# Performance work log

Measured on AMD Instinct MI355X. Metric: run time of the kernel, lower is better.

Reference implementation:

```python
import jax, jax.numpy as jnp
import numpy as np
from jax import lax

EPS = 1e-9

def _squash(v):
    # v: [..., D]; squash nonlinearity from CapsNet
    n = jnp.sum(jnp.square(v), axis=-1, keepdims=True)
    return (n / (1.0 + n) / jnp.sqrt(n + EPS)) * v

def setup_inputs() -> dict:
    key = jax.random.key(0)
    ks = jax.random.split(key, 12)
    B, S, D, NI = 1024, 200, 64, 4
    N_UID, N_MID = 50000, 100000
    return {
        "uid": jax.random.randint(ks[0], (B,), 0, N_UID, dtype=jnp.int32),
        "age": jax.random.randint(ks[1], (B,), 0, N_UID, dtype=jnp.int32),
        "gender": jax.random.randint(ks[2], (B,), 0, N_UID, dtype=jnp.int32),
        "occup": jax.random.randint(ks[3], (B,), 0, N_UID, dtype=jnp.int32),
        "mid_his": jax.random.randint(ks[4], (B, S), 0, N_MID, dtype=jnp.int32),
        "mask": jax.random.randint(ks[5], (B, S), 0, 2).astype(jnp.float32),
        "user_emb_table": jax.random.normal(ks[6], (N_UID, D), jnp.float32) * 0.1,
        "age_table": jax.random.normal(ks[7], (N_UID, D), jnp.float32) * 0.1,
        "gender_table": jax.random.normal(ks[8], (N_UID, D), jnp.float32) * 0.1,
        "occup_table": jax.random.normal(ks[9], (N_UID, D), jnp.float32) * 0.1,
        "mid_emb_table": jax.random.normal(ks[10], (N_MID, D), jnp.float32) * 0.1,
        "w_capsule": jax.random.normal(ks[11], (S, NI * D, D), jnp.float32),
    }

def reference(uid, age, gender, occup, mid_his, mask,
              user_emb_table, age_table, gender_table, occup_table,
              mid_emb_table, w_capsule):
    NI = 4
    B, S = mid_his.shape
    D = mid_emb_table.shape[1]

    # user profile: mean of 4 stacked user feature embeddings
    user_profile = (user_emb_table[uid] + gender_table[gender]
                    + age_table[age] + occup_table[occup]) * 0.25  # [B,D]

    # masked item history embeddings
    item_his = mid_emb_table[mid_his] * mask[:, :, None]  # [B,S,D]

    # adjacency: sigmoid(sum_d h_i[d]*h_j[d]*u[d]) without [B,S,S,D] blowup
    hu = item_his * user_profile[:, None, :]              # [B,S,D]
    adj = jax.nn.sigmoid(jnp.einsum('bid,bjd->bij', hu, item_his))  # [B,S,S]
    adj = adj * mask[:, None, :] * mask[:, :, None]

    # --- CapsuleNetwork, bilinear_type=2 ---
    # TF: sum(w[1,S,NI*D,D] * u[B,S,1,D], axis=3) == contraction over D
    hat = jnp.einsum('bsd,sed->bse', item_his, w_capsule)  # [B,S,NI*D]
    hat = hat.reshape(B, S, NI, D).transpose(0, 2, 1, 3)   # [B,NI,S,D]
    hat_iter = lax.stop_gradient(hat)

    cw = jnp.zeros((B, NI, S), dtype=item_his.dtype)  # routing logits
    atten_mask = mask[:, None, :]                     # [B,1,S] broadcast over NI
    for i in range(3):
        sw = jax.nn.softmax(cw, axis=1)               # softmax over interests
        sw = jnp.where(atten_mask == 0, 0.0, sw)      # [B,NI,S]
        if i < 2:
            cap = _squash(jnp.einsum('bks,bksd->bkd', sw, hat_iter))  # [B,NI,D]
            delta = jnp.einsum('bksd,bkd->bks', hat_iter, cap)
            cw = cw + delta
        else:
            cap = _squash(jnp.einsum('bks,bksd->bkd', sw, hat))
    interest_capsule = cap  # [B,NI,D]; relu_layer=False -> no projection
    return interest_capsule, adj
```

## Files before the change

### kernel.cpp

```cpp
#include <hip/hip_runtime.h>

#define B_SZ 1024
#define S_SZ 200
#define D_SZ 64
#define NI_SZ 4
#define E_SZ 256

using u16 = unsigned short;
using u32 = unsigned int;
typedef short  sh4    __attribute__((ext_vector_type(4)));
typedef short  sh8    __attribute__((ext_vector_type(8)));
typedef __bf16 bf16x8 __attribute__((ext_vector_type(8)));
typedef float  f32x4  __attribute__((ext_vector_type(4)));

__device__ __forceinline__ u16 f2bf(float x) {
  u32 u = __float_as_uint(x);
  u += 0x7FFFu + ((u >> 16) & 1u);
  return (u16)(u >> 16);
}
__device__ __forceinline__ float bf2f(u16 h) {
  return __uint_as_float(((u32)h) << 16);
}
__device__ __forceinline__ sh8 ldsr(const u16* arr, int row, int kshort) {
  const int idx = row * 64 + (kshort ^ ((row & 7) << 3));
  return *(const sh8*)(arr + idx);
}
__device__ __forceinline__ bf16x8 ldsw(const u16* arr, int row, int kshort) {
  return __builtin_bit_cast(bf16x8, ldsr(arr, row, kshort));
}
__device__ __forceinline__ void stsw(u16* arr, int row, int c, sh8 v) {
  *(sh8*)(arr + row * 64 + 8 * (c ^ (row & 7))) = v;
}
__device__ __forceinline__ sh8 cvt8(const float* __restrict__ src, float m) {
  const float4 a = *(const float4*)(src);
  const float4 d = *(const float4*)(src + 4);
  sh8 v;
  v[0] = (short)f2bf(a.x * m); v[1] = (short)f2bf(a.y * m);
  v[2] = (short)f2bf(a.z * m); v[3] = (short)f2bf(a.w * m);
  v[4] = (short)f2bf(d.x * m); v[5] = (short)f2bf(d.y * m);
  v[6] = (short)f2bf(d.z * m); v[7] = (short)f2bf(d.w * m);
  return v;
}

__global__ __launch_bounds__(256) void adj_kernel(
    const int* __restrict__ uid, const int* __restrict__ age,
    const int* __restrict__ gender, const int* __restrict__ occup,
    const float* __restrict__ U, const float* __restrict__ AT,
    const float* __restrict__ GT, const float* __restrict__ OT,
    const int* __restrict__ mid_his, const float* __restrict__ mask,
    const float* __restrict__ memb, float* __restrict__ adj)
{
  const int b = blockIdx.x;
  __shared__ u16   Hs[208 * 64];
  __shared__ float Ms[208];
  __shared__ int   midS[S_SZ];
  __shared__ float pS[D_SZ];
  const int tid = threadIdx.x;

  if (tid < 208) Ms[tid] = (tid < S_SZ) ? mask[b * S_SZ + tid] : 0.f;
  if (tid < S_SZ) midS[tid] = mid_his[b * S_SZ + tid];
  if (tid < D_SZ) {
    float v = U[(size_t)uid[b]     * D_SZ + tid]
            + GT[(size_t)gender[b] * D_SZ + tid]
            + AT[(size_t)age[b]    * D_SZ + tid]
            + OT[(size_t)occup[b]  * D_SZ + tid];
    pS[tid] = 0.25f * v;
  }
  __syncthreads();

  for (int idx = tid; idx < S_SZ * 8; idx += 256) {
    const int row = idx >> 3, c = idx & 7;
    const float m = Ms[row];
    sh8 v = {0, 0, 0, 0, 0, 0, 0, 0};
    if (m != 0.f) v = cvt8(memb + (size_t)midS[row] * D_SZ + c * 8, m);
    stsw(Hs, row, c, v);
  }
  if (tid < 64) {
    sh8 z = {0,0,0,0,0,0,0,0};
    stsw(Hs, S_SZ + (tid >> 3), tid & 7, z);
  }
  __syncthreads();

  const int w = tid >> 6, l = tid & 63;
  const int lr = l & 15, lg = l >> 4;
  float pvA[8], pvB[8];
  #pragma unroll
  for (int j = 0; j < 8; j++) { pvA[j] = pS[lg * 8 + j]; pvB[j] = pS[32 + lg * 8 + j]; }

  float* outb = adj + (size_t)b * S_SZ * S_SZ;
  for (int mt = 0; mt < 13; mt++) {
    const int arow = mt * 16 + lr;
    const sh8 r0 = ldsr(Hs, arow, lg * 8);
    const sh8 r1 = ldsr(Hs, arow, 32 + lg * 8);
    sh8 h0, h1;
    #pragma unroll
    for (int j = 0; j < 8; j++) {
      h0[j] = (short)f2bf(bf2f((u16)r0[j]) * pvA[j]);
      h1[j] = (short)f2bf(bf2f((u16)r1[j]) * pvB[j]);
    }
    const bf16x8 a0 = __builtin_bit_cast(bf16x8, h0);
    const bf16x8 a1 = __builtin_bit_cast(bf16x8, h1);
    for (int nt = w; nt < 13; nt += 4) {
      const int brow = nt * 16 + lr;
      const bf16x8 b0 = ldsw(Hs, brow, lg * 8);
      const bf16x8 b1 = ldsw(Hs, brow, 32 + lg * 8);
      f32x4 acc = {0.f, 0.f, 0.f, 0.f};
      acc = __builtin_amdgcn_mfma_f32_16x16x32_bf16(a0, b0, acc, 0, 0, 0);
      acc = __builtin_amdgcn_mfma_f32_16x16x32_bf16(a1, b1, acc, 0, 0, 0);
      const int n = nt * 16 + lr;
      const float mj = Ms[n];
      #pragma unroll
      for (int rr = 0; rr < 4; rr++) {
        const int m = mt * 16 + lg * 4 + rr;
        if (m < S_SZ && n < S_SZ) {
          const float sg = 1.f / (1.f + __expf(-acc[rr]));
          outb[(size_t)m * S_SZ + n] = sg * Ms[m] * mj;
        }
      }
    }
  }
}

__global__ __launch_bounds__(256, 6) void hat_kernel(
    const int* __restrict__ mid_his, const float* __restrict__ mask,
    const float* __restrict__ memb, const float* __restrict__ WC,
    u16* __restrict__ hatb)
{
  const int bid = blockIdx.x;
  const int s  = (bid >> 8) * 8 + (bid & 7);
  const int eh = (bid >> 3) & 1;
  const int b0 = ((bid >> 4) & 15) * 64;
  __shared__ u16 As[64 * 64];
  __shared__ u16 Ws_[128 * 64];
  __shared__ float mskS[64];
  const int tid = threadIdx.x;

  for (int idx = tid; idx < 64 * 8; idx += 256) {
    const int row = idx >> 3, c = idx & 7;
    const int bb = b0 + row;
    const float m = mask[bb * S_SZ + s];
    if (c == 0) mskS[row] = m;
    sh8 v = {0, 0, 0, 0, 0, 0, 0, 0};
    if (m != 0.f)
      v = cvt8(memb + (size_t)mid_his[bb * S_SZ + s] * D_SZ + c * 8, m);
    stsw(As, row, c, v);
  }
  for (int idx = tid; idx < 128 * 8; idx += 256) {
    const int row = idx >> 3, c = idx & 7;
    stsw(Ws_, row, c, cvt8(WC + ((size_t)s * E_SZ + eh * 128 + row) * D_SZ + c * 8, 1.f));
  }
  __syncthreads();

  const int w = tid >> 6, l = tid & 63;
  const int lr = l & 15, lg = l >> 4;

  f32x4 acc[2][4];
  #pragma unroll
  for (int me = 0; me < 2; me++)
    #pragma unroll
    for (int nb = 0; nb < 4; nb++) acc[me][nb] = (f32x4){0.f, 0.f, 0.f, 0.f};

  #pragma unroll
  for (int ks = 0; ks < 2; ks++) {
    bf16x8 wf[2], itf[4];
    #pragma unroll
    for (int me = 0; me < 2; me++)
      wf[me] = ldsw(Ws_, w * 32 + me * 16 + lr, ks * 32 + lg * 8);
    #pragma unroll
    for (int nb = 0; nb < 4; nb++)
      itf[nb] = ldsw(As, nb * 16 + lr, ks * 32 + lg * 8);
    #pragma unroll
    for (int me = 0; me < 2; me++)
      #pragma unroll
      for (int nb = 0; nb < 4; nb++)
        acc[me][nb] = __builtin_amdgcn_mfma_f32_16x16x32_bf16(wf[me], itf[nb], acc[me][nb], 0, 0, 0);
  }

  #pragma unroll
  for (int nb = 0; nb < 4; nb++) {
    const int bb = b0 + nb * 16 + lr;
    const bool live = (mskS[nb * 16 + lr] != 0.f);
    #pragma unroll
    for (int me = 0; me < 2; me++) {
      const int eg = eh * 128 + w * 32 + me * 16;
      const int kc = eg >> 6;
      const int d0 = (eg & 63) + lg * 4;
      if (live) {
        sh4 v;
        v[0] = (short)f2bf(acc[me][nb][0]);
        v[1] = (short)f2bf(acc[me][nb][1]);
        v[2] = (short)f2bf(acc[me][nb][2]);
        v[3] = (short)f2bf(acc[me][nb][3]);
        *(sh4*)(hatb + (((size_t)bb * NI_SZ + kc) * S_SZ + s) * D_SZ + d0) = v;
      }
    }
  }
}

__device__ __forceinline__ float rlane(float v, int l) {
  return __int_as_float(__builtin_amdgcn_readlane(__float_as_int(v), l));
}

__global__ __launch_bounds__(1024, 4) void route_kernel(
    const u16* __restrict__ hatb, const float* __restrict__ mask,
    float* __restrict__ out)
{
  const int b = blockIdx.x;
  const int t = threadIdx.x;
  const int w = t >> 6, lane = t & 63;
  const int k = w >> 2, q = w & 3;
  __shared__ float cwS[NI_SZ][212];
  __shared__ float partS[NI_SZ][4][D_SZ];

  const float msv = (lane < 50) ? mask[b * S_SZ + q * 50 + lane] : 0.f;

  float hr[50];
  const u16* hg = hatb + (((size_t)b * NI_SZ + k) * S_SZ + q * 50) * D_SZ + lane;
  #pragma unroll
  for (int j = 0; j < 50; j++) {
    const float hm = rlane(msv, j);
    const u16* p = (hm != 0.f) ? (hg + j * D_SZ) : hg;
    const float v = bf2f(*p);
    hr[j] = (hm != 0.f) ? v : 0.f;
  }
  #pragma unroll
  for (int j = 0; j < 50; j++) asm volatile("" : "+v"(hr[j]));

  const int jj = __brev(lane) >> 26;

  for (int iter = 0; iter < 3; ++iter) {
    float swv;
    if (iter == 0) {
      swv = 0.25f * msv;
    } else {
      const int sidx = q * 50 + (lane < 50 ? lane : 49);
      const float a0 = cwS[0][sidx], a1 = cwS[1][sidx],
                  a2 = cwS[2][sidx], a3 = cwS[3][sidx];
      const float mx = fmaxf(fmaxf(a0, a1), fmaxf(a2, a3));
      const float e0 = __expf(a0 - mx), e1 = __expf(a1 - mx),
                  e2 = __expf(a2 - mx), e3 = __expf(a3 - mx);
      const float ek = (k == 0) ? e0 : (k == 1) ? e1 : (k == 2) ? e2 : e3;
      const float inv = 1.f / (e0 + e1 + e2 + e3);
      swv = (msv == 0.f) ? 0.f : ek * inv;
    }

    float c0 = 0.f, c1 = 0.f, c2 = 0.f, c3 = 0.f;
    #pragma unroll
    for (int j = 0; j < 48; j += 4) {
      c0 = fmaf(rlane(swv, j + 0), hr[j + 0], c0);
      c1 = fmaf(rlane(swv, j + 1), hr[j + 1], c1);
      c2 = fmaf(rlane(swv, j + 2), hr[j + 2], c2);
      c3 = fmaf(rlane(swv, j + 3), hr[j + 3], c3);
    }
    c0 = fmaf(rlane(swv, 48), hr[48], c0);
    c1 = fmaf(rlane(swv, 49), hr[49], c1);
    partS[k][q][lane] = (c0 + c2) + (c1 + c3);
    __syncthreads();

    const float cap = partS[k][0][lane] + partS[k][1][lane]
                    + partS[k][2][lane] + partS[k][3][lane];
    float n = cap * cap;
    #pragma unroll
    for (int off = 32; off; off >>= 1) n += __shfl_xor(n, off);
    const float f = n / (1.f + n) * rsqrtf(n + 1e-9f);
    const float capd = cap * f;

    if (iter < 2) {
      float p[32];
      {
        const int bit = lane & 1;
        #pragma unroll
        for (int j = 0; j < 32; j++) {
          const float lo = hr[j] * capd;
          const float hi = (j + 32 < 50) ? hr[j + 32] * capd : 0.f;
          const float send = bit ? lo : hi;
          const float keep = bit ? hi : lo;
          p[j] = keep + __shfl_xor(send, 1);
        }
      }
      #pragma unroll
      for (int rr = 1; rr < 6; rr++) {
        const int dist = 1 << rr;
        const int half = 32 >> rr;
        const int bit = (lane >> rr) & 1;
        #pragma unroll
        for (int j = 0; j < 32; j++) {
          if (j < half) {
            const float send = bit ? p[j] : p[j + half];
            const float keep = bit ? p[j + half] : p[j];
            p[j] = keep + __shfl_xor(send, dist);
          }
        }
      }
      if (jj < 50) {
        if (iter == 0) cwS[k][q * 50 + jj] = p[0];
        else           cwS[k][q * 50 + jj] += p[0];
      }
      __syncthreads();
    } else if (q == 0) {
      out[((size_t)b * NI_SZ + k) * D_SZ + lane] = capd;
    }
  }
}

extern "C" void kernel_launch(void* const* d_in, const int* in_sizes, int n_in,
                              void* d_out, int out_size, void* d_ws, size_t ws_size,
                              hipStream_t stream)
{
  const int*   uid     = (const int*)d_in[0];
  const int*   age     = (const int*)d_in[1];
  const int*   gender  = (const int*)d_in[2];
  const int*   occup   = (const int*)d_in[3];
  const int*   mid_his = (const int*)d_in[4];
  const float* mask    = (const float*)d_in[5];
  const float* U       = (const float*)d_in[6];
  const float* AT      = (const float*)d_in[7];
  const float* GT      = (const float*)d_in[8];
  const float* OT      = (const float*)d_in[9];
  const float* ME      = (const float*)d_in[10];
  const float* WC      = (const float*)d_in[11];

  float* out  = (float*)d_out;
  float* adj  = out + B_SZ * NI_SZ * D_SZ;

  u16* hatb = (u16*)d_ws;

  adj_kernel<<<B_SZ, 256, 0, stream>>>(uid, age, gender, occup, U, AT, GT, OT,
                                       mid_his, mask, ME, adj);
  hat_kernel<<<6400, 256, 0, stream>>>(mid_his, mask, ME, WC, hatb);
  route_kernel<<<B_SZ, 1024, 0, stream>>>(hatb, mask, out);
}
```

Baseline: 136.3 us.

## Compact live columns in adj kernel and stage output rows through LDS

Builds a compacted list of unmasked history positions with ballot/popcount, and computes the adjacency MFMA tiles only over live columns. Masked columns are known to be zero. Results are scattered into an LDS row buffer and written out as coalesced float4 rows, with the buffer zeroed after each write-out. This cuts MFMA and sigmoid work roughly in half for the 50% mask and replaces strided scalar global stores with vectorized ones. In exchange it adds two block barriers per 8-row chunk plus extra LDS traffic.

```diff
diff --git a/kernel.cpp b/kernel.cpp
--- a/kernel.cpp
+++ b/kernel.cpp
@@ -55,6 +55,9 @@
   __shared__ float Ms[208];
   __shared__ int   midS[S_SZ];
   __shared__ float pS[D_SZ];
+  __shared__ u16   liveS[208];
+  __shared__ int   Lsh;
+  __shared__ float OutS[8 * 212];
   const int tid = threadIdx.x;
 
   if (tid < 208) Ms[tid] = (tid < S_SZ) ? mask[b * S_SZ + tid] : 0.f;
@@ -66,8 +69,23 @@
             + OT[(size_t)occup[b]  * D_SZ + tid];
     pS[tid] = 0.25f * v;
   }
+  if (tid < 208) liveS[tid] = 207;
+  for (int i = tid; i < 8 * 212; i += 256) OutS[i] = 0.f;
   __syncthreads();
 
+  if (tid < 64) {
+    int base = 0;
+    #pragma unroll
+    for (int c = 0; c < 4; c++) {
+      const int s = c * 64 + tid;
+      const bool live = (s < S_SZ) && (Ms[s] != 0.f);
+      const unsigned long long mk = __ballot(live);
+      const int pfx = __popcll(mk & ((1ull << tid) - 1ull));
+      if (live) liveS[base + pfx] = (u16)s;
+      base += (int)__popcll(mk);
+    }
+    if (tid == 0) Lsh = base;
+  }
   for (int idx = tid; idx < S_SZ * 8; idx += 256) {
     const int row = idx >> 3, c = idx & 7;
     const float m = Ms[row];
@@ -81,6 +99,8 @@
   }
   __syncthreads();
 
+  const int L   = Lsh;
+  const int nTc = (L + 15) >> 4;
   const int w = tid >> 6, l = tid & 63;
   const int lr = l & 15, lg = l >> 4;
   float pvA[8], pvB[8];
@@ -88,6 +108,7 @@
   for (int j = 0; j < 8; j++) { pvA[j] = pS[lg * 8 + j]; pvB[j] = pS[32 + lg * 8 + j]; }
 
   float* outb = adj + (size_t)b * S_SZ * S_SZ;
+
   for (int mt = 0; mt < 13; mt++) {
     const int arow = mt * 16 + lr;
     const sh8 r0 = ldsr(Hs, arow, lg * 8);
@@ -100,23 +121,59 @@
     }
     const bf16x8 a0 = __builtin_bit_cast(bf16x8, h0);
     const bf16x8 a1 = __builtin_bit_cast(bf16x8, h1);
-    for (int nt = w; nt < 13; nt += 4) {
-      const int brow = nt * 16 + lr;
-      const bf16x8 b0 = ldsw(Hs, brow, lg * 8);
-      const bf16x8 b1 = ldsw(Hs, brow, 32 + lg * 8);
-      f32x4 acc = {0.f, 0.f, 0.f, 0.f};
-      acc = __builtin_amdgcn_mfma_f32_16x16x32_bf16(a0, b0, acc, 0, 0, 0);
-      acc = __builtin_amdgcn_mfma_f32_16x16x32_bf16(a1, b1, acc, 0, 0, 0);
-      const int n = nt * 16 + lr;
-      const float mj = Ms[n];
-      #pragma unroll
-      for (int rr = 0; rr < 4; rr++) {
-        const int m = mt * 16 + lg * 4 + rr;
-        if (m < S_SZ && n < S_SZ) {
+
+    float msm[4];
+    #pragma unroll
+    for (int rr = 0; rr < 4; rr++) msm[rr] = Ms[mt * 16 + lg * 4 + rr];
+
+    f32x4 ov[4];
+    int   jv[4];
+    #pragma unroll
+    for (int t = 0; t < 4; t++) {
+      const int ntc = w + t * 4;
+      jv[t] = 207;
+      ov[t] = (f32x4){0.f, 0.f, 0.f, 0.f};
+      if (ntc < nTc) {
+        const int jr = liveS[ntc * 16 + lr];
+        jv[t] = jr;
+        const bf16x8 b0 = ldsw(Hs, jr, lg * 8);
+        const bf16x8 b1 = ldsw(Hs, jr, 32 + lg * 8);
+        f32x4 acc = {0.f, 0.f, 0.f, 0.f};
+        acc = __builtin_amdgcn_mfma_f32_16x16x32_bf16(a0, b0, acc, 0, 0, 0);
+        acc = __builtin_amdgcn_mfma_f32_16x16x32_bf16(a1, b1, acc, 0, 0, 0);
+        const float mj = Ms[jr];
+        #pragma unroll
+        for (int rr = 0; rr < 4; rr++) {
           const float sg = 1.f / (1.f + __expf(-acc[rr]));
-          outb[(size_t)m * S_SZ + n] = sg * Ms[m] * mj;
-        }
-      }
+          ov[t][rr] = sg * msm[rr] * mj;
+        }
+      }
+    }
+
+    #pragma unroll
+    for (int h = 0; h < 2; h++) {
+      if ((lg >> 1) == h) {
+        #pragma unroll
+        for (int t = 0; t < 4; t++) {
+          if (w + t * 4 < nTc) {
+            #pragma unroll
+            for (int rr = 0; rr < 4; rr++)
+              OutS[((lg & 1) * 4 + rr) * 212 + jv[t]] = ov[t][rr];
+          }
+        }
+      }
+      __syncthreads();
+      const int rowbase = mt * 16 + h * 8;
+      if (rowbase < S_SZ) {
+        for (int c = tid; c < 400; c += 256) {
+          const int r = c / 50, cc = (c % 50) * 4;
+          float4* ls = (float4*)&OutS[r * 212 + cc];
+          const float4 v = *ls;
+          *(float4*)&outb[(size_t)(rowbase + r) * S_SZ + cc] = v;
+          *ls = make_float4(0.f, 0.f, 0.f, 0.f);
+        }
+      }
+      __syncthreads();
     }
   }
 }
```

Result: no change. 136.0 us (-0.2%).
